# Performance work log

Hardware: AMD Instinct MI355X
Metric: run time of the kernel (lower is better)

## Reference

```python
import jax, jax.numpy as jnp
import numpy as np


def conv1x1(x, w, b):
    # x: [B,C,H,W], w: [O,C], b: [O]
    return jnp.einsum('bchw,oc->bohw', x, w) + b[None, :, None, None]


def resize_bilinear(x, h, w):
    # matches torch F.interpolate(mode='bilinear', align_corners=False), no antialias
    B, C = x.shape[:2]
    return jax.image.resize(x, (B, C, h, w), method='bilinear', antialias=False)


def attend(q_map, k_map, v_map, num_heads, scale):
    # q_map/k_map/v_map: [B, hidden, H, W] -> out [B, hidden, H, W]
    B, D, H, W = q_map.shape
    hd = D // num_heads
    N = H * W
    q = q_map.reshape(B, num_heads, hd, N).transpose(0, 1, 3, 2)  # [B,h,N,d]
    k = k_map.reshape(B, num_heads, hd, N)                         # [B,h,d,N]
    v = v_map.reshape(B, num_heads, hd, N).transpose(0, 1, 3, 2)  # [B,h,N,d]
    scores = jnp.einsum('bhnd,bhdm->bhnm', q, k) * scale
    attn = jax.nn.softmax(scores, axis=-1)
    out = jnp.einsum('bhnm,bhmd->bhnd', attn, v)                   # [B,h,N,d]
    return out.transpose(0, 1, 3, 2).reshape(B, D, H, W)


NUM_HEADS = 8
HIDDEN = 256
HEAD_DIM = HIDDEN // NUM_HEADS
SCALE = HEAD_DIM ** -0.5


def setup_inputs() -> dict:
    key = jax.random.key(0)
    ks = jax.random.split(key, 20)
    C_h, C_l = 128, 256
    inp = {
        'high_feat': jax.random.normal(ks[0], (2, C_h, 64, 64), jnp.float32),
        'low_feat': jax.random.normal(ks[1], (2, C_l, 32, 32), jnp.float32),
    }
    def lin(k, o, c):
        kw, kb = jax.random.split(k)
        s = 1.0 / np.sqrt(c)
        return (jax.random.uniform(kw, (o, c), jnp.float32, -s, s),
                jax.random.uniform(kb, (o,), jnp.float32, -s, s))
    inp['q_high_w'], inp['q_high_b'] = lin(ks[2], HIDDEN, C_h)
    inp['k_high_w'], inp['k_high_b'] = lin(ks[3], HIDDEN, C_h)
    inp['v_high_w'], inp['v_high_b'] = lin(ks[4], HIDDEN, C_h)
    inp['q_low_w'], inp['q_low_b'] = lin(ks[5], HIDDEN, C_l)
    inp['k_low_w'], inp['k_low_b'] = lin(ks[6], HIDDEN, C_l)
    inp['v_low_w'], inp['v_low_b'] = lin(ks[7], HIDDEN, C_l)
    inp['out_high_w'], inp['out_high_b'] = lin(ks[8], C_h, HIDDEN)
    inp['out_low_w'], inp['out_low_b'] = lin(ks[9], C_l, HIDDEN)
    return inp


def reference(high_feat, low_feat,
              q_high_w, q_high_b, k_high_w, k_high_b, v_high_w, v_high_b,
              q_low_w, q_low_b, k_low_w, k_low_b, v_low_w, v_low_b,
              out_high_w, out_high_b, out_low_w, out_low_b):
    B, C_h, H, W = high_feat.shape
    _, C_l, Hl, Wl = low_feat.shape

    # high queries attend to upsampled-low keys/values
    low_up = resize_bilinear(low_feat, H, W)
    q_h = conv1x1(high_feat, q_high_w, q_high_b)
    k_l = conv1x1(low_up, k_low_w, k_low_b)
    v_l = conv1x1(low_up, v_low_w, v_low_b)
    high_out = attend(q_h, k_l, v_l, NUM_HEADS, SCALE)
    high_out = conv1x1(high_out, out_high_w, out_high_b)

    # low queries attend to downsampled-high keys/values
    q_l = conv1x1(low_feat, q_low_w, q_low_b)
    k_h = resize_bilinear(conv1x1(high_feat, k_high_w, k_high_b), Hl, Wl)
    v_h = resize_bilinear(conv1x1(high_feat, v_high_w, v_high_b), Hl, Wl)
    low_out = attend(q_l, k_h, v_h, NUM_HEADS, SCALE)
    low_out = conv1x1(low_out, out_low_w, out_low_b)

    return (high_out, low_out)
```

## Files before the change

kernel.cpp:

```cpp
#include <hip/hip_runtime.h>
#include <hip/hip_bf16.h>

#define HEADS 8
#define HD    32

typedef __attribute__((ext_vector_type(8))) short short8;
typedef __attribute__((ext_vector_type(4))) float f32x4;
typedef unsigned short us;

__device__ __forceinline__ us f2bf(float f) {
  union { __hip_bfloat16 h; us u; } cv;
  cv.h = __float2bfloat16(f);
  return cv.u;
}
__device__ __forceinline__ float bf2f(us u) {
  union { float f; unsigned int i; } cv;
  cv.i = ((unsigned int)u) << 16;
  return cv.f;
}
__device__ __forceinline__ float exp2_native(float x) {
  float r;
  asm("v_exp_f32 %0, %1" : "=v"(r) : "v"(x));
  return r;
}
__device__ __forceinline__ void glds16(const us* g, us* l) {
  __builtin_amdgcn_global_load_lds(
      (const __attribute__((address_space(1))) void*)g,
      (__attribute__((address_space(3))) void*)l, 16, 0, 0);
}

struct GP {
  const void* X;
  const float* den;
  const float* W; const float* bias; void* out;
  int C, O, N, omode, xmode, nsp; float alpha;
};

template<int XMODE, int NSP>
__device__ __forceinline__ void gemm_body(const GP& g, int bid,
                                          us* Wh, us* Wl, us* Xh, us* Xl) {
  const int C = g.C, O = g.O, N = g.N;
  int nx = N >> 6, nyo = O >> 6;
  int b = bid / (nx * nyo);
  int rr = bid - b * (nx * nyo);
  int o0 = (rr / nx) << 6;
  int n0 = (rr - (rr / nx) * nx) << 6;

  int tid = threadIdx.x, w = tid >> 6, l = tid & 63, lq = l & 15, l4 = l >> 4;

  int wr = tid >> 2, wcb = tid & 3;
  int xn = tid & 63, xcg = tid >> 6;
  const float* Wp = g.W + (size_t)(o0 + wr) * C + wcb * 8;
  const float* Xf = (const float*)g.X;
  size_t xbase = (size_t)b * C * N + n0 + xn;
  int wof = wr * 32 + ((wcb ^ ((wr >> 1) & 3)) << 3);
  int xof = xn * 32 + ((xcg ^ ((xn >> 1) & 3)) << 3);

  auto stage = [&](int s, int bufi) {
    int c0 = s << 5;
    float4 wa = *(const float4*)(Wp + c0);
    float4 wb = *(const float4*)(Wp + c0 + 4);
    float wv[8] = {wa.x, wa.y, wa.z, wa.w, wb.x, wb.y, wb.z, wb.w};
    short8 whv, wlv;
#pragma unroll
    for (int j = 0; j < 8; ++j) {
      us h = f2bf(wv[j]);
      whv[j] = (short)h;
      wlv[j] = (short)f2bf(wv[j] - bf2f(h));
    }
    *(short8*)&Wh[bufi * 2048 + wof] = whv;
    *(short8*)&Wl[bufi * 2048 + wof] = wlv;
    float inv = 0.f;
    if constexpr (XMODE == 2) {
      size_t doff = ((size_t)(b * 8 + (c0 >> 5))) * N + n0 + xn;
      float dsum = 0.f;
#pragma unroll
      for (int s2 = 0; s2 < NSP; ++s2) dsum += g.den[(size_t)s2 * 16 * N + doff];
      inv = 1.f / dsum;
    }
    short8 xhv, xlv;
#pragma unroll
    for (int j = 0; j < 8; ++j) {
      int c = c0 + xcg * 8 + j;
      float xv;
      if constexpr (XMODE == 0) {
        xv = Xf[xbase + (size_t)c * N];
      } else if constexpr (XMODE == 2) {
        xv = 0.f;
#pragma unroll
        for (int s2 = 0; s2 < NSP; ++s2)
          xv += Xf[(size_t)s2 * 512 * N + xbase + (size_t)c * N];
        xv *= inv;
      } else {
        int n = n0 + xn, yy = n >> 5, xx = (n & 31) << 1;
        const float* hp = Xf + ((size_t)(b * C + c)) * 4096 + yy * 128 + xx;
        xv = 0.25f * (hp[0] + hp[1] + hp[64] + hp[65]);
      }
      us h = f2bf(xv);
      xhv[j] = (short)h;
      xlv[j] = (short)f2bf(xv - bf2f(h));
    }
    *(short8*)&Xh[bufi * 2048 + xof] = xhv;
    *(short8*)&Xl[bufi * 2048 + xof] = xlv;
  };

  f32x4 acc[4] = {{0,0,0,0},{0,0,0,0},{0,0,0,0},{0,0,0,0}};
  int ns = C >> 5, cur = 0;
  stage(0, 0);
  for (int s = 0; s < ns; ++s) {
    __syncthreads();
    if (s + 1 < ns) stage(s + 1, cur ^ 1);
    int swz = (l4 ^ ((lq >> 1) & 3)) << 3;
    int arow = w * 16 + lq;
    short8 ah = *(const short8*)&Wh[cur * 2048 + arow * 32 + swz];
    short8 al = *(const short8*)&Wl[cur * 2048 + arow * 32 + swz];
    __builtin_amdgcn_s_setprio(1);
#pragma unroll
    for (int nf = 0; nf < 4; ++nf) {
      int brow = nf * 16 + lq;
      short8 bh = *(const short8*)&Xh[cur * 2048 + brow * 32 + swz];
      short8 bl = *(const short8*)&Xl[cur * 2048 + brow * 32 + swz];
      acc[nf] = __builtin_amdgcn_mfma_f32_16x16x32_bf16(ah, bh, acc[nf], 0, 0, 0);
      acc[nf] = __builtin_amdgcn_mfma_f32_16x16x32_bf16(ah, bl, acc[nf], 0, 0, 0);
      acc[nf] = __builtin_amdgcn_mfma_f32_16x16x32_bf16(al, bh, acc[nf], 0, 0, 0);
    }
    __builtin_amdgcn_s_setprio(0);
    cur ^= 1;
  }

  float bv[4];
#pragma unroll
  for (int r = 0; r < 4; ++r) bv[r] = g.bias[o0 + w * 16 + l4 * 4 + r];
  if (g.omode == 0) {
    us* ob = (us*)g.out;
#pragma unroll
    for (int nf = 0; nf < 4; ++nf) {
      ushort4 pk;
      pk.x = f2bf((acc[nf][0] + bv[0]) * g.alpha);
      pk.y = f2bf((acc[nf][1] + bv[1]) * g.alpha);
      pk.z = f2bf((acc[nf][2] + bv[2]) * g.alpha);
      pk.w = f2bf((acc[nf][3] + bv[3]) * g.alpha);
      *(ushort4*)&ob[((size_t)b * N + n0 + nf * 16 + lq) * O + o0 + w * 16 + l4 * 4] = pk;
    }
  } else if (g.omode == 1) {
    us* ob = (us*)g.out;
#pragma unroll
    for (int nf = 0; nf < 4; ++nf)
#pragma unroll
      for (int r = 0; r < 4; ++r)
        ob[((size_t)(b * O + o0 + w * 16 + l4 * 4 + r)) * N + n0 + nf * 16 + lq] =
            f2bf(acc[nf][r] + bv[r]);
  } else {
    float* of = (float*)g.out;
#pragma unroll
    for (int nf = 0; nf < 4; ++nf)
#pragma unroll
      for (int r = 0; r < 4; ++r)
        of[((size_t)(b * O + o0 + w * 16 + l4 * 4 + r)) * N + n0 + nf * 16 + lq] =
            acc[nf][r] + bv[r];
  }
}

__global__ __launch_bounds__(256) void gemm_conv(
    GP g0, GP g1, GP g2, GP g3, GP g4, GP g5,
    int nb0, int nb1, int nb2, int nb3, int nb4) {
  __shared__ __align__(16) us Wh[2 * 2048], Wl[2 * 2048];
  __shared__ __align__(16) us Xh[2 * 2048], Xl[2 * 2048];
  int bid = blockIdx.x;
  GP g;
  if (bid < nb0) g = g0;
  else if (bid < nb0 + nb1) { g = g1; bid -= nb0; }
  else if (bid < nb0 + nb1 + nb2) { g = g2; bid -= nb0 + nb1; }
  else if (bid < nb0 + nb1 + nb2 + nb3) { g = g3; bid -= nb0 + nb1 + nb2; }
  else if (bid < nb0 + nb1 + nb2 + nb3 + nb4) { g = g4; bid -= nb0 + nb1 + nb2 + nb3; }
  else { g = g5; bid -= nb0 + nb1 + nb2 + nb3 + nb4; }
  if (g.xmode == 0)      gemm_body<0, 1>(g, bid, Wh, Wl, Xh, Xl);
  else if (g.xmode == 3) gemm_body<3, 1>(g, bid, Wh, Wl, Xh, Xl);
  else                   gemm_body<2, 2>(g, bid, Wh, Wl, Xh, Xl);
}

__global__ __launch_bounds__(256) void upsample_both(
    const us* __restrict__ inT, us* __restrict__ outT,
    const us* __restrict__ inC, us* __restrict__ outC, int nbT, int BC) {
  if ((int)blockIdx.x < nbT) {
    int rowg = blockIdx.x * 4 + (threadIdx.x >> 6);
    int ch = (threadIdx.x & 63) * 4;
    int b = rowg >> 12, n = rowg & 4095;
    int y = n >> 6, x = n & 63;
    float sy = y * 0.5f - 0.25f, sx = x * 0.5f - 0.25f;
    int y0 = (int)floorf(sy), x0 = (int)floorf(sx);
    float fy = sy - (float)y0, fx = sx - (float)x0;
    int y0c = max(y0, 0), y1c = min(y0 + 1, 31);
    int x0c = max(x0, 0), x1c = min(x0 + 1, 31);
    const us* ip = inT + (size_t)b * 1024 * 256 + ch;
    ushort4 v00 = *(const ushort4*)&ip[(size_t)(y0c * 32 + x0c) * 256];
    ushort4 v01 = *(const ushort4*)&ip[(size_t)(y0c * 32 + x1c) * 256];
    ushort4 v10 = *(const ushort4*)&ip[(size_t)(y1c * 32 + x0c) * 256];
    ushort4 v11 = *(const ushort4*)&ip[(size_t)(y1c * 32 + x1c) * 256];
    float w00 = (1.f - fy) * (1.f - fx), w01 = (1.f - fy) * fx;
    float w10 = fy * (1.f - fx), w11 = fy * fx;
    ushort4 o;
    o.x = f2bf(w00 * bf2f(v00.x) + w01 * bf2f(v01.x) + w10 * bf2f(v10.x) + w11 * bf2f(v11.x));
    o.y = f2bf(w00 * bf2f(v00.y) + w01 * bf2f(v01.y) + w10 * bf2f(v10.y) + w11 * bf2f(v11.y));
    o.z = f2bf(w00 * bf2f(v00.z) + w01 * bf2f(v01.z) + w10 * bf2f(v10.z) + w11 * bf2f(v11.z));
    o.w = f2bf(w00 * bf2f(v00.w) + w01 * bf2f(v01.w) + w10 * bf2f(v10.w) + w11 * bf2f(v11.w));
    *(ushort4*)&outT[((size_t)b * 4096 + n) * 256 + ch] = o;
  } else {
    int t = ((int)blockIdx.x - nbT) * 256 + threadIdx.x;
    if (t >= BC * 64) return;
    int y = t & 63, bc = t >> 6;
    float sy = y * 0.5f - 0.25f;
    int y0 = (int)floorf(sy);
    float fy = sy - (float)y0;
    int y0c = max(y0, 0), y1c = min(y0 + 1, 31);
    const us* r0 = inC + (size_t)bc * 1024 + y0c * 32;
    const us* r1 = inC + (size_t)bc * 1024 + y1c * 32;
    float m[32];
#pragma unroll
    for (int j = 0; j < 32; j += 8) {
      short8 a = *(const short8*)(r0 + j);
      short8 c = *(const short8*)(r1 + j);
#pragma unroll
      for (int e = 0; e < 8; ++e)
        m[j + e] = (1.f - fy) * bf2f((us)a[e]) + fy * bf2f((us)c[e]);
    }
    us* op = outC + (size_t)bc * 4096 + y * 64;
    short8 o8;
#pragma unroll
    for (int xo = 0; xo < 64; ++xo) {
      int k = xo >> 1;
      float v;
      if (xo & 1) v = (k < 31) ? 0.75f * m[k] + 0.25f * m[k + 1] : m[31];
      else        v = (k > 0) ? 0.25f * m[k - 1] + 0.75f * m[k] : m[0];
      o8[xo & 7] = (short)f2bf(v);
      if ((xo & 7) == 7) *(short8*)(op + (xo & ~7)) = o8;
    }
  }
}

__global__ __launch_bounds__(256) void attn_mfma(
    const us* __restrict__ qT0, const us* __restrict__ kT0,
    const us* __restrict__ vC0, float* __restrict__ pn0, float* __restrict__ pd0,
    int N0, int nb0, int nsp0,
    const us* __restrict__ qT1, const us* __restrict__ kT1,
    const us* __restrict__ vC1, float* __restrict__ pn1, float* __restrict__ pd1,
    int N1, int nsp1) {
  __shared__ __align__(16) us Kt[2][64 * 32];
  __shared__ __align__(16) us Vt[2][32 * 64];
  __shared__ __align__(16) us Pt[8][16 * 64];

  int bid = blockIdx.x;
  const us *qT, *kT, *vC; float *pn, *pd; int N, nsp;
  if (bid < nb0) {
    qT = qT0; kT = kT0; vC = vC0; pn = pn0; pd = pd0; N = N0; nsp = nsp0;
  } else {
    bid -= nb0;
    qT = qT1; kT = kT1; vC = vC1; pn = pn1; pd = pd1; N = N1; nsp = nsp1;
  }
  int xcd = bid & 7, slot = bid >> 3;
  int nqb = N >> 7, per = nqb * nsp;
  int qs = slot % per;
  int bh = ((slot / per) << 3) | xcd;
  int qb = qs / nsp, sp = qs % nsp;
  int b = bh >> 3, h = bh & 7;
  int SK = N / nsp;
  int tid = threadIdx.x;
  int w = tid >> 6, l = tid & 63;
  int lq = l & 15, l4 = l >> 4;

  short8 qfrag[2];
#pragma unroll
  for (int g = 0; g < 2; ++g) {
    const us* qp = qT + ((size_t)(b * N + qb * 128 + g * 64 + w * 16 + lq)) * 256 +
                   h * 32 + l4 * 8;
    qfrag[g] = *(const short8*)qp;
  }

  int rK = w * 16 + (l >> 2);
  const us* gK = kT + ((size_t)(b * N + sp * SK + rK)) * 256 + h * 32 +
                 (((l & 3) ^ ((rK >> 1) & 3)) << 3);
  int dV = w * 8 + (l >> 3);
  const us* gV = vC + ((size_t)(b * 256 + h * 32 + dV)) * N + sp * SK +
                 (((l & 7) ^ (dV & 7)) << 3);

  f32x4 acc0[2] = {{0,0,0,0},{0,0,0,0}};
  f32x4 acc1[2] = {{0,0,0,0},{0,0,0,0}};
  f32x4 acc2[2] = {{0,0,0,0},{0,0,0,0}};
  short8 ones;
#pragma unroll
  for (int j = 0; j < 8; ++j) ones[j] = (short)0x3F80;

  glds16(gK, &Kt[0][w * 512]);
  glds16(gV, &Vt[0][w * 512]);

  int nt = SK >> 6, cur = 0;
  for (int t = 0; t < nt; ++t) {
    __syncthreads();
    if (t + 1 < nt) {
      glds16(gK + (size_t)(t + 1) * 64 * 256, &Kt[cur ^ 1][w * 512]);
      glds16(gV + (t + 1) * 64, &Vt[cur ^ 1][w * 512]);
    }
    const us* Kb = Kt[cur];
    const us* Vb = Vt[cur];

#pragma unroll
    for (int kg = 0; kg < 4; ++kg) {
      int key = kg * 16 + lq;
      short8 a = *(const short8*)&Kb[key * 32 + ((l4 ^ ((key >> 1) & 3)) << 3)];
      f32x4 zero = {0.f, 0.f, 0.f, 0.f};
      int key0 = kg * 16 + l4 * 4;
      int pof = lq * 64 + (((key0 >> 3) ^ (lq & 7)) << 3) + (key0 & 7);
#pragma unroll
      for (int g = 0; g < 2; ++g) {
        __builtin_amdgcn_s_setprio(1);
        f32x4 s = __builtin_amdgcn_mfma_f32_16x16x32_bf16(a, qfrag[g], zero, 0, 0, 0);
        __builtin_amdgcn_s_setprio(0);
        float p0 = exp2_native(s[0]);
        float p1 = exp2_native(s[1]);
        float p2 = exp2_native(s[2]);
        float p3 = exp2_native(s[3]);
        unsigned int r01, r23;
        asm("v_cvt_pk_bf16_f32 %0, %1, %2" : "=v"(r01) : "v"(p0), "v"(p1));
        asm("v_cvt_pk_bf16_f32 %0, %1, %2" : "=v"(r23) : "v"(p2), "v"(p3));
        uint2 pk; pk.x = r01; pk.y = r23;
        *(uint2*)&Pt[w * 2 + g][pof] = pk;
      }
    }

#pragma unroll
    for (int kh = 0; kh < 2; ++kh) {
      int d0 = lq, d1 = 16 + lq;
      short8 vf0 = *(const short8*)&Vb[d0 * 64 + (((kh * 4 + l4) ^ (d0 & 7)) << 3)];
      short8 vf1 = *(const short8*)&Vb[d1 * 64 + (((kh * 4 + l4) ^ (d1 & 7)) << 3)];
      int pof = lq * 64 + (((kh * 4 + l4) ^ (lq & 7)) << 3);
#pragma unroll
      for (int g = 0; g < 2; ++g) {
        short8 pfr = *(const short8*)&Pt[w * 2 + g][pof];
        __builtin_amdgcn_s_setprio(1);
        acc0[g] = __builtin_amdgcn_mfma_f32_16x16x32_bf16(vf0, pfr, acc0[g], 0, 0, 0);
        acc1[g] = __builtin_amdgcn_mfma_f32_16x16x32_bf16(vf1, pfr, acc1[g], 0, 0, 0);
        acc2[g] = __builtin_amdgcn_mfma_f32_16x16x32_bf16(ones, pfr, acc2[g], 0, 0, 0);
        __builtin_amdgcn_s_setprio(0);
      }
    }
    cur ^= 1;
  }

  size_t nbase = ((size_t)((sp * 2 + b) * 8 + h)) * 32 * N;
  size_t dbase = ((size_t)((sp * 2 + b) * 8 + h)) * N;
#pragma unroll
  for (int g = 0; g < 2; ++g) {
    int q = qb * 128 + g * 64 + w * 16 + lq;
#pragma unroll
    for (int r = 0; r < 4; ++r) {
      pn[nbase + (size_t)(l4 * 4 + r) * N + q] = acc0[g][r];
      pn[nbase + (size_t)(16 + l4 * 4 + r) * N + q] = acc1[g][r];
    }
    if (l4 == 0) pd[dbase + q] = acc2[g][0];
  }
}

extern "C" void kernel_launch(void* const* d_in, const int* in_sizes, int n_in,
                              void* d_out, int out_size, void* d_ws, size_t ws_size,
                              hipStream_t stream) {
  const float* high_feat  = (const float*)d_in[0];
  const float* low_feat   = (const float*)d_in[1];
  const float* q_high_w   = (const float*)d_in[2];
  const float* q_high_b   = (const float*)d_in[3];
  const float* k_high_w   = (const float*)d_in[4];
  const float* k_high_b   = (const float*)d_in[5];
  const float* v_high_w   = (const float*)d_in[6];
  const float* v_high_b   = (const float*)d_in[7];
  const float* q_low_w    = (const float*)d_in[8];
  const float* q_low_b    = (const float*)d_in[9];
  const float* k_low_w    = (const float*)d_in[10];
  const float* k_low_b    = (const float*)d_in[11];
  const float* v_low_w    = (const float*)d_in[12];
  const float* v_low_b    = (const float*)d_in[13];
  const float* out_high_w = (const float*)d_in[14];
  const float* out_high_b = (const float*)d_in[15];
  const float* out_low_w  = (const float*)d_in[16];
  const float* out_low_b  = (const float*)d_in[17];

  const int B = 2, Nh = 4096, Nl = 1024;
  const float qa = 0.17677669529663689f * 1.4426950408889634f;

  char* p = (char*)d_ws;
  us* qT    = (us*)p; p += (size_t)2 * 4096 * 256 * 2;
  us* kTb   = (us*)p; p += (size_t)2 * 4096 * 256 * 2;
  us* vCb   = (us*)p; p += (size_t)2 * 256 * 4096 * 2;
  us* klbT  = (us*)p; p += (size_t)2 * 1024 * 256 * 2;
  us* vlb   = (us*)p; p += (size_t)2 * 256 * 1024 * 2;
  us* qTl   = (us*)p; p += (size_t)2 * 1024 * 256 * 2;
  us* kTl   = (us*)p; p += (size_t)2 * 1024 * 256 * 2;
  us* vCl   = (us*)p; p += (size_t)2 * 256 * 1024 * 2;
  float* pnH = (float*)p; p += (size_t)2 * 16 * 32 * 4096 * 4;
  float* pdH = (float*)p; p += (size_t)2 * 16 * 4096 * 4;
  float* pnL = (float*)p; p += (size_t)2 * 16 * 32 * 1024 * 4;
  float* pdL = (float*)p; p += (size_t)2 * 16 * 1024 * 4;

  float* out_high = (float*)d_out;
  float* out_low  = out_high + 2 * 128 * 4096;

  GP z = {nullptr, nullptr, nullptr, nullptr, nullptr, 32, 64, 64, 2, 0, 1, 0.f};

  {
    GP s0 = {low_feat,  nullptr, k_low_w,  k_low_b,  klbT, 256, 256, Nl, 0, 0, 1, 1.0f};
    GP s1 = {low_feat,  nullptr, v_low_w,  v_low_b,  vlb,  256, 256, Nl, 1, 0, 1, 1.0f};
    GP s2 = {high_feat, nullptr, q_high_w, q_high_b, qT,   128, 256, Nh, 0, 0, 1, qa};
    GP s3 = {low_feat,  nullptr, q_low_w,  q_low_b,  qTl,  256, 256, Nl, 0, 0, 1, qa};
    GP s4 = {high_feat, nullptr, k_high_w, k_high_b, kTl,  128, 256, Nl, 0, 3, 1, 1.0f};
    GP s5 = {high_feat, nullptr, v_high_w, v_high_b, vCl,  128, 256, Nl, 1, 3, 1, 1.0f};
    gemm_conv<<<1152, 256, 0, stream>>>(s0, s1, s2, s3, s4, s5, 128, 128, 512, 128, 128);
  }
  upsample_both<<<2048 + 128, 256, 0, stream>>>(klbT, kTb, vlb, vCb, 2048, B * 256);
  {
    int nb0 = 16 * (Nh / 128) * 2, nb1 = 16 * (Nl / 128) * 2;
    attn_mfma<<<nb0 + nb1, 256, 0, stream>>>(
        qT, kTb, vCb, pnH, pdH, Nh, nb0, 2,
        qTl, kTl, vCl, pnL, pdL, Nl, 2);
  }
  {
    GP s0 = {pnH, pdH, out_high_w, out_high_b, out_high, 256, 128, Nh, 2, 2, 2, 1.0f};
    GP s1 = {pnL, pdL, out_low_w,  out_low_b,  out_low,  256, 256, Nl, 2, 2, 2, 1.0f};
    gemm_conv<<<384, 256, 0, stream>>>(s0, s1, z, z, z, z, 256, 128, 0, 0, 0);
  }
}
```

Baseline: 102.1 us.

## Use 32x32x16 MFMA with permlane32 swap to keep P in registers

```diff
diff --git a/kernel.cpp b/kernel.cpp
--- a/kernel.cpp
+++ b/kernel.cpp
@@ -6,6 +6,7 @@
 
 typedef __attribute__((ext_vector_type(8))) short short8;
 typedef __attribute__((ext_vector_type(4))) float f32x4;
+typedef __attribute__((ext_vector_type(16))) float f32x16;
 typedef unsigned short us;
 
 __device__ __forceinline__ us f2bf(float f) {
@@ -247,7 +248,6 @@
     int N1, int nsp1) {
   __shared__ __align__(16) us Kt[2][64 * 32];
   __shared__ __align__(16) us Vt[2][32 * 64];
-  __shared__ __align__(16) us Pt[8][16 * 64];
 
   int bid = blockIdx.x;
   const us *qT, *kT, *vC; float *pn, *pd; int N, nsp;
@@ -266,14 +266,14 @@
   int SK = N / nsp;
   int tid = threadIdx.x;
   int w = tid >> 6, l = tid & 63;
-  int lq = l & 15, l4 = l >> 4;
-
-  short8 qfrag[2];
-#pragma unroll
-  for (int g = 0; g < 2; ++g) {
-    const us* qp = qT + ((size_t)(b * N + qb * 128 + g * 64 + w * 16 + lq)) * 256 +
-                   h * 32 + l4 * 8;
-    qfrag[g] = *(const short8*)qp;
+  int q5 = l & 31, hi = l >> 5;
+
+  short8 qf0, qf1;
+  {
+    const us* qp = qT + ((size_t)(b * N + qb * 128 + w * 32 + q5)) * 256 +
+                   h * 32 + hi * 8;
+    qf0 = *(const short8*)qp;
+    qf1 = *(const short8*)(qp + 16);
   }
 
   int rK = w * 16 + (l >> 2);
@@ -283,9 +283,8 @@
   const us* gV = vC + ((size_t)(b * 256 + h * 32 + dV)) * N + sp * SK +
                  (((l & 7) ^ (dV & 7)) << 3);
 
-  f32x4 acc0[2] = {{0,0,0,0},{0,0,0,0}};
-  f32x4 acc1[2] = {{0,0,0,0},{0,0,0,0}};
-  f32x4 acc2[2] = {{0,0,0,0},{0,0,0,0}};
+  f32x16 acc = {0.f};
+  f32x16 accD = {0.f};
   short8 ones;
 #pragma unroll
   for (int j = 0; j < 8; ++j) ones[j] = (short)0x3F80;
@@ -304,60 +303,58 @@
     const us* Vb = Vt[cur];
 
 #pragma unroll
-    for (int kg = 0; kg < 4; ++kg) {
-      int key = kg * 16 + lq;
-      short8 a = *(const short8*)&Kb[key * 32 + ((l4 ^ ((key >> 1) & 3)) << 3)];
-      f32x4 zero = {0.f, 0.f, 0.f, 0.f};
-      int key0 = kg * 16 + l4 * 4;
-      int pof = lq * 64 + (((key0 >> 3) ^ (lq & 7)) << 3) + (key0 & 7);
-#pragma unroll
-      for (int g = 0; g < 2; ++g) {
-        __builtin_amdgcn_s_setprio(1);
-        f32x4 s = __builtin_amdgcn_mfma_f32_16x16x32_bf16(a, qfrag[g], zero, 0, 0, 0);
-        __builtin_amdgcn_s_setprio(0);
-        float p0 = exp2_native(s[0]);
-        float p1 = exp2_native(s[1]);
-        float p2 = exp2_native(s[2]);
-        float p3 = exp2_native(s[3]);
-        unsigned int r01, r23;
-        asm("v_cvt_pk_bf16_f32 %0, %1, %2" : "=v"(r01) : "v"(p0), "v"(p1));
-        asm("v_cvt_pk_bf16_f32 %0, %1, %2" : "=v"(r23) : "v"(p2), "v"(p3));
-        uint2 pk; pk.x = r01; pk.y = r23;
-        *(uint2*)&Pt[w * 2 + g][pof] = pk;
+    for (int grp = 0; grp < 2; ++grp) {
+      int kr = grp * 32 + q5;
+      short8 ka = *(const short8*)&Kb[kr * 32 + ((hi ^ ((kr >> 1) & 3)) << 3)];
+      short8 kb2 = *(const short8*)&Kb[kr * 32 + (((2 + hi) ^ ((kr >> 1) & 3)) << 3)];
+      f32x16 s = {0.f};
+      __builtin_amdgcn_s_setprio(1);
+      s = __builtin_amdgcn_mfma_f32_32x32x16_bf16(ka, qf0, s, 0, 0, 0);
+      s = __builtin_amdgcn_mfma_f32_32x32x16_bf16(kb2, qf1, s, 0, 0, 0);
+      __builtin_amdgcn_s_setprio(0);
+
+      unsigned int u[8];
+#pragma unroll
+      for (int i = 0; i < 8; ++i) {
+        float pa = exp2_native(s[2 * i]);
+        float pb = exp2_native(s[2 * i + 1]);
+        asm("v_cvt_pk_bf16_f32 %0, %1, %2" : "=v"(u[i]) : "v"(pa), "v"(pb));
       }
-    }
-
-#pragma unroll
-    for (int kh = 0; kh < 2; ++kh) {
-      int d0 = lq, d1 = 16 + lq;
-      short8 vf0 = *(const short8*)&Vb[d0 * 64 + (((kh * 4 + l4) ^ (d0 & 7)) << 3)];
-      short8 vf1 = *(const short8*)&Vb[d1 * 64 + (((kh * 4 + l4) ^ (d1 & 7)) << 3)];
-      int pof = lq * 64 + (((kh * 4 + l4) ^ (lq & 7)) << 3);
-#pragma unroll
-      for (int g = 0; g < 2; ++g) {
-        short8 pfr = *(const short8*)&Pt[w * 2 + g][pof];
-        __builtin_amdgcn_s_setprio(1);
-        acc0[g] = __builtin_amdgcn_mfma_f32_16x16x32_bf16(vf0, pfr, acc0[g], 0, 0, 0);
-        acc1[g] = __builtin_amdgcn_mfma_f32_16x16x32_bf16(vf1, pfr, acc1[g], 0, 0, 0);
-        acc2[g] = __builtin_amdgcn_mfma_f32_16x16x32_bf16(ones, pfr, acc2[g], 0, 0, 0);
-        __builtin_amdgcn_s_setprio(0);
+      asm volatile("v_permlane32_swap_b32 %0, %1" : "+v"(u[0]), "+v"(u[2]));
+      asm volatile("v_permlane32_swap_b32 %0, %1" : "+v"(u[1]), "+v"(u[3]));
+      asm volatile("v_permlane32_swap_b32 %0, %1" : "+v"(u[4]), "+v"(u[6]));
+      asm volatile("v_permlane32_swap_b32 %0, %1" : "+v"(u[5]), "+v"(u[7]));
+      short8 pfA, pfB;
+      {
+        union { unsigned int w2[4]; short8 s8; } cvA, cvB;
+        cvA.w2[0] = u[0]; cvA.w2[1] = u[1]; cvA.w2[2] = u[2]; cvA.w2[3] = u[3];
+        cvB.w2[0] = u[4]; cvB.w2[1] = u[5]; cvB.w2[2] = u[6]; cvB.w2[3] = u[7];
+        pfA = cvA.s8; pfB = cvB.s8;
       }
+
+      int kb0 = grp * 4 + hi;
+      int kb1 = grp * 4 + 2 + hi;
+      short8 va = *(const short8*)&Vb[q5 * 64 + ((kb0 ^ (q5 & 7)) << 3)];
+      short8 vb = *(const short8*)&Vb[q5 * 64 + ((kb1 ^ (q5 & 7)) << 3)];
+      __builtin_amdgcn_s_setprio(1);
+      acc  = __builtin_amdgcn_mfma_f32_32x32x16_bf16(va, pfA, acc, 0, 0, 0);
+      accD = __builtin_amdgcn_mfma_f32_32x32x16_bf16(ones, pfA, accD, 0, 0, 0);
+      acc  = __builtin_amdgcn_mfma_f32_32x32x16_bf16(vb, pfB, acc, 0, 0, 0);
+      accD = __builtin_amdgcn_mfma_f32_32x32x16_bf16(ones, pfB, accD, 0, 0, 0);
+      __builtin_amdgcn_s_setprio(0);
     }
     cur ^= 1;
   }
 
   size_t nbase = ((size_t)((sp * 2 + b) * 8 + h)) * 32 * N;
   size_t dbase = ((size_t)((sp * 2 + b) * 8 + h)) * N;
-#pragma unroll
-  for (int g = 0; g < 2; ++g) {
-    int q = qb * 128 + g * 64 + w * 16 + lq;
-#pragma unroll
-    for (int r = 0; r < 4; ++r) {
-      pn[nbase + (size_t)(l4 * 4 + r) * N + q] = acc0[g][r];
-      pn[nbase + (size_t)(16 + l4 * 4 + r) * N + q] = acc1[g][r];
-    }
-    if (l4 == 0) pd[dbase + q] = acc2[g][0];
-  }
+  int qg = qb * 128 + w * 32 + q5;
+#pragma unroll
+  for (int r = 0; r < 16; ++r) {
+    int d = (r & 3) + 8 * (r >> 2) + 4 * hi;
+    pn[nbase + (size_t)d * N + qg] = acc[r];
+  }
+  if (hi == 0) pd[dbase + qg] = accD[0];
 }
 
 extern "C" void kernel_launch(void* const* d_in, const int* in_sizes, int n_in,
```

New measurement: 109.3 us. 7.1% more time.
